# Optimization experiments

Measured on AMD Instinct MI355X. Metric: run time of the kernel, lower is better.

Reference implementation:

```python
import jax, jax.numpy as jnp
import numpy as np

HEADS = 8


def setup_inputs() -> dict:
    key = jax.random.key(0)
    ks = jax.random.split(key, 5)
    B, C, H, W = 4, 256, 48, 48
    x = jax.random.normal(ks[0], (B, C, H, W), dtype=jnp.float32)
    # 1x1 conv weights == channel matmul matrices
    w_qkv = jax.random.normal(ks[1], (3 * C, C), dtype=jnp.float32) * (C ** -0.5)
    b_qkv = jax.random.normal(ks[2], (3 * C,), dtype=jnp.float32) * 0.02
    w_proj = jax.random.normal(ks[3], (C, C), dtype=jnp.float32) * (C ** -0.5)
    b_proj = jax.random.normal(ks[4], (C,), dtype=jnp.float32) * 0.02
    return {"x": x, "w_qkv": w_qkv, "b_qkv": b_qkv, "w_proj": w_proj, "b_proj": b_proj}


def reference(x, w_qkv, b_qkv, w_proj, b_proj):
    B, C, H, W = x.shape
    heads = HEADS
    dh = C // heads
    HW = H * W
    scale = dh ** -0.5
    # qkv 1x1 conv: [B, 3C, H, W]
    qkv = jnp.einsum('bchw,oc->bohw', x, w_qkv) + b_qkv[None, :, None, None]
    # reshape(B,3,heads,dh,HW).transpose(-2,-1) -> [B,3,heads,HW,dh]
    qkv = qkv.reshape(B, 3, heads, dh, HW).transpose(0, 1, 2, 4, 3)
    q = qkv[:, 0] * scale  # [B,h,HW,dh]
    k = qkv[:, 1]
    v = qkv[:, 2]
    scores = jnp.einsum('bhnd,bhmd->bhnm', q, k)  # [B,h,HW,HW]
    scores = scores - jnp.max(scores, axis=-1, keepdims=True)
    exp_scores = jnp.exp(scores)
    weights = exp_scores / jnp.maximum(exp_scores.sum(axis=-1, keepdims=True), 1e-12)
    attn = jnp.einsum('bhnm,bhmd->bhnd', weights, v)  # [B,h,HW,dh]
    # transpose(2,3).reshape(B,C,H,W): [B,h,dh,HW] -> [B,C,H,W]
    attn = attn.transpose(0, 1, 3, 2).reshape(B, C, H, W)
    out = jnp.einsum('bchw,oc->bohw', attn, w_proj) + b_proj[None, :, None, None]
    return out
```

## Files before the change

kernel.cpp:

```cpp
#include <hip/hip_runtime.h>
#include <math.h>

#define HW 2304
#define QS 0.2550565355f

typedef _Float16 f16;
typedef __attribute__((ext_vector_type(4))) _Float16 f16x4;
typedef __attribute__((ext_vector_type(8))) _Float16 f16x8;
typedef __attribute__((ext_vector_type(4))) float f32x4;

#if __has_builtin(__builtin_amdgcn_exp2f)
#define EXP2F(x) __builtin_amdgcn_exp2f(x)
#else
#define EXP2F(x) exp2f(x)
#endif

static __device__ __forceinline__ f16x4 pack4(float a, float b, float c, float d) {
    auto lo = __builtin_amdgcn_cvt_pkrtz(a, b);
    auto hi = __builtin_amdgcn_cvt_pkrtz(c, d);
    f16x4 r;
    r[0] = (f16)lo[0]; r[1] = (f16)lo[1]; r[2] = (f16)hi[0]; r[3] = (f16)hi[1];
    return r;
}

__global__ __launch_bounds__(256) void cvt_w(const float* __restrict__ wq,
                                             const float* __restrict__ wp,
                                             f16* __restrict__ wh) {
    const int i = (blockIdx.x * 256 + threadIdx.x) * 4;
    float4 v;
    if (i < 768 * 256) v = *(const float4*)(wq + i);
    else               v = *(const float4*)(wp + (i - 768 * 256));
    f16x4 h = {(f16)v.x, (f16)v.y, (f16)v.z, (f16)v.w};
    *(f16x4*)(wh + i) = h;
}

__global__ __launch_bounds__(256) void cvt_x(const float* __restrict__ x,
                                             f16* __restrict__ xt) {
    __shared__ f16 tile[64][72];
    const int t  = threadIdx.x;
    const int n0 = blockIdx.x * 64, c0 = blockIdx.y * 64, b = blockIdx.z;
    const float* xb = x + ((size_t)b * 256 + c0) * HW + n0;
#pragma unroll
    for (int pass = 0; pass < 4; ++pass) {
        const int u  = t + pass * 256;
        const int cr = u >> 4, cc = u & 15;
        const float4 v = *(const float4*)(xb + (size_t)cr * HW + 4 * cc);
        tile[4 * cc + 0][cr] = (f16)v.x;
        tile[4 * cc + 1][cr] = (f16)v.y;
        tile[4 * cc + 2][cr] = (f16)v.z;
        tile[4 * cc + 3][cr] = (f16)v.w;
    }
    __syncthreads();
    f16* xo = xt + ((size_t)b * HW + n0) * 256 + c0;
#pragma unroll
    for (int pass = 0; pass < 2; ++pass) {
        const int u  = t + pass * 256;
        const int nr = u >> 3, nc = u & 7;
        *(f16x8*)(xo + (size_t)nr * 256 + 8 * nc) = *(const f16x8*)&tile[nr][8 * nc];
    }
}

__global__ __launch_bounds__(64) void qkv_gemm(const f16* __restrict__ xt,
                                               const f16* __restrict__ wh,
                                               const float* __restrict__ bias,
                                               f16* __restrict__ qt,
                                               f16* __restrict__ kt,
                                               f16* __restrict__ vn) {
    const int lane = threadIdx.x & 63;
    const int c    = lane & 15, q4 = lane >> 4;
    const int n0   = blockIdx.x * 64;
    const int m0   = blockIdx.y * 64;
    const int b    = blockIdx.z;
    const int s    = (blockIdx.x + blockIdx.y) & 7;
    const f16* xb  = xt + (size_t)b * HW * 256;

    f32x4 C[4][4] = {};
    f16x8 af[2][4], bf[2][4];
    const int k0 = s * 32;
#pragma unroll
    for (int mt = 0; mt < 4; ++mt)
        af[0][mt] = *(const f16x8*)(wh + (size_t)(m0 + mt * 16 + c) * 256 + k0 + q4 * 8);
#pragma unroll
    for (int nt = 0; nt < 4; ++nt)
        bf[0][nt] = *(const f16x8*)(xb + (size_t)(n0 + nt * 16 + c) * 256 + k0 + q4 * 8);

#pragma unroll
    for (int it = 0; it < 8; ++it) {
        const int p = it & 1, pn = p ^ 1;
        const int kn = ((s + it + 1) & 7) * 32;
#pragma unroll
        for (int mt = 0; mt < 4; ++mt)
            af[pn][mt] = *(const f16x8*)(wh + (size_t)(m0 + mt * 16 + c) * 256 + kn + q4 * 8);
#pragma unroll
        for (int nt = 0; nt < 4; ++nt)
            bf[pn][nt] = *(const f16x8*)(xb + (size_t)(n0 + nt * 16 + c) * 256 + kn + q4 * 8);
#pragma unroll
        for (int mt = 0; mt < 4; ++mt)
#pragma unroll
            for (int nt = 0; nt < 4; ++nt)
                C[mt][nt] = __builtin_amdgcn_mfma_f32_16x16x32_f16(af[p][mt], bf[p][nt], C[mt][nt], 0, 0, 0);
    }

#pragma unroll
    for (int mt = 0; mt < 4; ++mt) {
        const int od = m0 + mt * 16 + q4 * 4;
        const float4 bv = *(const float4*)(bias + od);
        const int seg = od >> 8;
        const int oo  = od & 255;
        const int h   = oo >> 5, d0 = oo & 31;
        const size_t bh = (size_t)b * 8 + h;
#pragma unroll
        for (int nt = 0; nt < 4; ++nt) {
            const int n = n0 + nt * 16 + c;
            float v0 = C[mt][nt][0] + bv.x;
            float v1 = C[mt][nt][1] + bv.y;
            float v2 = C[mt][nt][2] + bv.z;
            float v3 = C[mt][nt][3] + bv.w;
            if (seg == 0) {
                v0 *= QS; v1 *= QS; v2 *= QS; v3 *= QS;
                f16x4 hv = {(f16)v0, (f16)v1, (f16)v2, (f16)v3};
                *(f16x4*)(qt + (bh * HW + n) * 32 + d0) = hv;
            } else if (seg == 1) {
                f16x4 hv = {(f16)v0, (f16)v1, (f16)v2, (f16)v3};
                *(f16x4*)(kt + (bh * HW + n) * 32 + d0) = hv;
            } else {
                const int nsw = n0 + (c >> 2) * 16 + nt * 4 + (c & 3);
                vn[(bh * 32 + d0 + 0) * HW + nsw] = (f16)v0;
                vn[(bh * 32 + d0 + 1) * HW + nsw] = (f16)v1;
                vn[(bh * 32 + d0 + 2) * HW + nsw] = (f16)v2;
                vn[(bh * 32 + d0 + 3) * HW + nsw] = (f16)v3;
            }
        }
    }
}

__global__ __launch_bounds__(256, 3) void attn_kernel(const f16* __restrict__ qt,
                                                      const f16* __restrict__ kt,
                                                      const f16* __restrict__ vn,
                                                      f16* __restrict__ at) {
    __shared__ float ored[2][96][36];
    __shared__ float lred[2][96];

    const int t    = threadIdx.x;
    const int lane = t & 63;
    const int w    = t >> 6;
    const int gh   = w >> 1;
    const int jh   = w & 1;
    const int c    = lane & 15, q4 = lane >> 4;
    const int bhid = blockIdx.x;
    const int h    = bhid & 7, b = bhid >> 3;
    const int i0   = blockIdx.y * 96;
    const size_t bh = (size_t)b * 8 + h;

    const f16* qtb = qt + bh * (size_t)HW * 32;
    const f16* kb = kt + bh * (size_t)HW * 32 + (size_t)(jh * 1152 + c) * 32 + q4 * 8;
    const f16* vb = vn + bh * (size_t)32 * HW + (size_t)c * HW + jh * 1152 + q4 * 16;

    f16x8 qf[3];
#pragma unroll
    for (int g = 0; g < 3; ++g)
        qf[g] = *(const f16x8*)(qtb + (size_t)(i0 + gh * 48 + g * 16 + c) * 32 + q4 * 8);

    const f16 oneh = (f16)(c == 0 ? 1.0f : 0.0f);
    const f16x4 ones = {oneh, oneh, oneh, oneh};

    f32x4 O[3][2] = {};
    f32x4 lacc[3] = {};

    f16x8 kA[4], kB[4];
    f16x4 vA[2][4], vB[2][4];

#define LOADK(dst, j) {                                                        \
        const f16* p_ = kb + (size_t)(j) * 32;                                 \
        dst[0] = *(const f16x8*)(p_);                                          \
        dst[1] = *(const f16x8*)(p_ + 512);                                    \
        dst[2] = *(const f16x8*)(p_ + 1024);                                   \
        dst[3] = *(const f16x8*)(p_ + 1536);                                   \
    }
#define LOADV(dst, j) {                                                        \
        const f16* p_ = vb + (j);                                              \
        *(f16x8*)&dst[0][0] = *(const f16x8*)(p_);                             \
        *(f16x8*)&dst[0][2] = *(const f16x8*)(p_ + 8);                         \
        *(f16x8*)&dst[1][0] = *(const f16x8*)(p_ + 16 * HW);                   \
        *(f16x8*)&dst[1][2] = *(const f16x8*)(p_ + 16 * HW + 8);               \
    }
#define COMPUTE(kf, vv) {                                                      \
        const f32x4 z_ = {0.f, 0.f, 0.f, 0.f};                                 \
        _Pragma("unroll")                                                      \
        for (int t4 = 0; t4 < 4; ++t4) {                                       \
            f16x4 P[3];                                                        \
            _Pragma("unroll")                                                  \
            for (int g = 0; g < 3; ++g) {                                      \
                const f32x4 S = __builtin_amdgcn_mfma_f32_16x16x32_f16(        \
                    kf[t4], qf[g], z_, 0, 0, 0);                               \
                P[g] = pack4(EXP2F(S[0]), EXP2F(S[1]), EXP2F(S[2]),            \
                             EXP2F(S[3]));                                     \
            }                                                                  \
            _Pragma("unroll")                                                  \
            for (int g = 0; g < 3; ++g) {                                      \
                O[g][0] = __builtin_amdgcn_mfma_f32_16x16x16f16(               \
                    vv[0][t4], P[g], O[g][0], 0, 0, 0);                        \
                O[g][1] = __builtin_amdgcn_mfma_f32_16x16x16f16(               \
                    vv[1][t4], P[g], O[g][1], 0, 0, 0);                        \
                lacc[g] = __builtin_amdgcn_mfma_f32_16x16x16f16(               \
                    ones, P[g], lacc[g], 0, 0, 0);                             \
            }                                                                  \
        }                                                                      \
    }

    LOADK(kA, 0);
    LOADV(vA, 0);
#pragma unroll 1
    for (int s = 0; s < 9; ++s) {
        const int j1 = s * 128 + 64;
        const int j2 = (s == 8) ? 0 : j1 + 64;
        LOADK(kB, j1);
        LOADV(vB, j1);
        COMPUTE(kA, vA);
        LOADK(kA, j2);
        LOADV(vA, j2);
        COMPUTE(kB, vB);
    }
#undef LOADK
#undef LOADV
#undef COMPUTE

#pragma unroll
    for (int g = 0; g < 3; ++g) {
        const int row = gh * 48 + g * 16 + c;
#pragma unroll
        for (int dh = 0; dh < 2; ++dh)
            *(f32x4*)&ored[jh][row][dh * 16 + q4 * 4] = O[g][dh];
        if (q4 == 0) lred[jh][row] = lacc[g][0];
    }
    __syncthreads();

    if (t < 192) {
        const int i   = t >> 1;
        const int d16 = (t & 1) * 16;
        const float l = lred[0][i] + lred[1][i];
        const float inv = 1.f / fmaxf(l, 1e-12f);
        float4 s[4];
#pragma unroll
        for (int k = 0; k < 4; ++k) {
            const float4 pa = *(const float4*)&ored[0][i][d16 + 4 * k];
            const float4 pb = *(const float4*)&ored[1][i][d16 + 4 * k];
            s[k].x = pa.x + pb.x; s[k].y = pa.y + pb.y;
            s[k].z = pa.z + pb.z; s[k].w = pa.w + pb.w;
        }
        f16* op = at + ((size_t)b * HW + i0 + i) * 256 + h * 32 + d16;
        *(f16x4*)(op + 0)  = pack4(s[0].x * inv, s[0].y * inv, s[0].z * inv, s[0].w * inv);
        *(f16x4*)(op + 4)  = pack4(s[1].x * inv, s[1].y * inv, s[1].z * inv, s[1].w * inv);
        *(f16x4*)(op + 8)  = pack4(s[2].x * inv, s[2].y * inv, s[2].z * inv, s[2].w * inv);
        *(f16x4*)(op + 12) = pack4(s[3].x * inv, s[3].y * inv, s[3].z * inv, s[3].w * inv);
    }
}

__global__ __launch_bounds__(64) void proj_gemm(const f16* __restrict__ at,
                                                const f16* __restrict__ wh,
                                                const float* __restrict__ bias,
                                                float* __restrict__ out) {
    const int lane = threadIdx.x & 63;
    const int c    = lane & 15, q4 = lane >> 4;
    const int n0   = blockIdx.x * 64;
    const int m0   = blockIdx.y * 64;
    const int b    = blockIdx.z;
    const int s    = (blockIdx.x + blockIdx.y) & 7;
    const f16* ab  = at + (size_t)b * HW * 256;

    f32x4 C[4][4] = {};
    f16x8 af[2][4], bf[2][4];
    const int k0 = s * 32;
#pragma unroll
    for (int mt = 0; mt < 4; ++mt)
        af[0][mt] = *(const f16x8*)(wh + (size_t)(m0 + mt * 16 + c) * 256 + k0 + q4 * 8);
#pragma unroll
    for (int nt = 0; nt < 4; ++nt)
        bf[0][nt] = *(const f16x8*)(ab + (size_t)(n0 + nt * 16 + c) * 256 + k0 + q4 * 8);

#pragma unroll
    for (int it = 0; it < 8; ++it) {
        const int p = it & 1, pn = p ^ 1;
        const int kn = ((s + it + 1) & 7) * 32;
#pragma unroll
        for (int mt = 0; mt < 4; ++mt)
            af[pn][mt] = *(const f16x8*)(wh + (size_t)(m0 + mt * 16 + c) * 256 + kn + q4 * 8);
#pragma unroll
        for (int nt = 0; nt < 4; ++nt)
            bf[pn][nt] = *(const f16x8*)(ab + (size_t)(n0 + nt * 16 + c) * 256 + kn + q4 * 8);
#pragma unroll
        for (int mt = 0; mt < 4; ++mt)
#pragma unroll
            for (int nt = 0; nt < 4; ++nt)
                C[mt][nt] = __builtin_amdgcn_mfma_f32_16x16x32_f16(af[p][mt], bf[p][nt], C[mt][nt], 0, 0, 0);
    }

#pragma unroll
    for (int mt = 0; mt < 4; ++mt) {
        const int od = m0 + mt * 16 + q4 * 4;
        const float4 bv = *(const float4*)(bias + od);
#pragma unroll
        for (int nt = 0; nt < 4; ++nt) {
            const int n = n0 + nt * 16 + c;
            out[((size_t)b * 256 + od + 0) * HW + n] = C[mt][nt][0] + bv.x;
            out[((size_t)b * 256 + od + 1) * HW + n] = C[mt][nt][1] + bv.y;
            out[((size_t)b * 256 + od + 2) * HW + n] = C[mt][nt][2] + bv.z;
            out[((size_t)b * 256 + od + 3) * HW + n] = C[mt][nt][3] + bv.w;
        }
    }
}

extern "C" void kernel_launch(void* const* d_in, const int* in_sizes, int n_in,
                              void* d_out, int out_size, void* d_ws, size_t ws_size,
                              hipStream_t stream) {
    const float* x      = (const float*)d_in[0];
    const float* w_qkv  = (const float*)d_in[1];
    const float* b_qkv  = (const float*)d_in[2];
    const float* w_proj = (const float*)d_in[3];
    const float* b_proj = (const float*)d_in[4];
    float* out = (float*)d_out;

    const size_t per = (size_t)4 * HW * 256;
    f16* xt = (f16*)d_ws;
    f16* wh = xt + per;
    f16* qt = wh + 262144;
    f16* kt = qt + per;
    f16* vn = kt + per;
    f16* at = vn + per;

    cvt_w<<<256, 256, 0, stream>>>(w_qkv, w_proj, wh);
    cvt_x<<<dim3(36, 4, 4), 256, 0, stream>>>(x, xt);
    qkv_gemm<<<dim3(36, 12, 4), 64, 0, stream>>>(xt, wh, b_qkv, qt, kt, vn);
    attn_kernel<<<dim3(32, 24), 256, 0, stream>>>(qt, kt, vn, at);
    proj_gemm<<<dim3(36, 4, 4), 64, 0, stream>>>(at, wh + 768 * 256, b_proj, out);
}
```

Measured before the change: 144.0 us.

## Stage K/V tiles through LDS in attention; merge conversion kernels; drop k-rotation

In the attention kernel, the four waves cooperatively load K and V tiles into double-buffered shared memory instead of each wave reading its own copy straight from global memory. This removes redundant global loads across waves that share the same j-half. The cost is a barrier per tile and extra LDS traffic. The two fp32-to-fp16 conversion kernels are merged into one launch, and the staggered k-start rotation in the GEMMs is replaced by plain sequential k order.

```diff
diff --git a/kernel.cpp b/kernel.cpp
--- a/kernel.cpp
+++ b/kernel.cpp
@@ -23,22 +23,26 @@
     return r;
 }
 
-__global__ __launch_bounds__(256) void cvt_w(const float* __restrict__ wq,
-                                             const float* __restrict__ wp,
-                                             f16* __restrict__ wh) {
-    const int i = (blockIdx.x * 256 + threadIdx.x) * 4;
-    float4 v;
-    if (i < 768 * 256) v = *(const float4*)(wq + i);
-    else               v = *(const float4*)(wp + (i - 768 * 256));
-    f16x4 h = {(f16)v.x, (f16)v.y, (f16)v.z, (f16)v.w};
-    *(f16x4*)(wh + i) = h;
-}
-
-__global__ __launch_bounds__(256) void cvt_x(const float* __restrict__ x,
-                                             f16* __restrict__ xt) {
+__global__ __launch_bounds__(256) void cvt_all(const float* __restrict__ x,
+                                               const float* __restrict__ wq,
+                                               const float* __restrict__ wp,
+                                               f16* __restrict__ xt,
+                                               f16* __restrict__ wh) {
     __shared__ f16 tile[64][72];
-    const int t  = threadIdx.x;
-    const int n0 = blockIdx.x * 64, c0 = blockIdx.y * 64, b = blockIdx.z;
+    const int bid = blockIdx.x;
+    const int t   = threadIdx.x;
+    if (bid >= 576) {
+        const int i = ((bid - 576) * 256 + t) * 4;
+        float4 v;
+        if (i < 768 * 256) v = *(const float4*)(wq + i);
+        else               v = *(const float4*)(wp + (i - 768 * 256));
+        f16x4 h = {(f16)v.x, (f16)v.y, (f16)v.z, (f16)v.w};
+        *(f16x4*)(wh + i) = h;
+        return;
+    }
+    const int bx = bid % 36, rem = bid / 36;
+    const int by = rem & 3, bz = rem >> 2;
+    const int n0 = bx * 64, c0 = by * 64, b = bz;
     const float* xb = x + ((size_t)b * 256 + c0) * HW + n0;
 #pragma unroll
     for (int pass = 0; pass < 4; ++pass) {
@@ -71,23 +75,21 @@
     const int n0   = blockIdx.x * 64;
     const int m0   = blockIdx.y * 64;
     const int b    = blockIdx.z;
-    const int s    = (blockIdx.x + blockIdx.y) & 7;
     const f16* xb  = xt + (size_t)b * HW * 256;
 
     f32x4 C[4][4] = {};
     f16x8 af[2][4], bf[2][4];
-    const int k0 = s * 32;
 #pragma unroll
     for (int mt = 0; mt < 4; ++mt)
-        af[0][mt] = *(const f16x8*)(wh + (size_t)(m0 + mt * 16 + c) * 256 + k0 + q4 * 8);
+        af[0][mt] = *(const f16x8*)(wh + (size_t)(m0 + mt * 16 + c) * 256 + q4 * 8);
 #pragma unroll
     for (int nt = 0; nt < 4; ++nt)
-        bf[0][nt] = *(const f16x8*)(xb + (size_t)(n0 + nt * 16 + c) * 256 + k0 + q4 * 8);
+        bf[0][nt] = *(const f16x8*)(xb + (size_t)(n0 + nt * 16 + c) * 256 + q4 * 8);
 
 #pragma unroll
     for (int it = 0; it < 8; ++it) {
         const int p = it & 1, pn = p ^ 1;
-        const int kn = ((s + it + 1) & 7) * 32;
+        const int kn = (it == 7) ? 0 : (it + 1) * 32;
 #pragma unroll
         for (int mt = 0; mt < 4; ++mt)
             af[pn][mt] = *(const f16x8*)(wh + (size_t)(m0 + mt * 16 + c) * 256 + kn + q4 * 8);
@@ -138,14 +140,17 @@
                                                       const f16* __restrict__ kt,
                                                       const f16* __restrict__ vn,
                                                       f16* __restrict__ at) {
-    __shared__ float ored[2][96][36];
-    __shared__ float lred[2][96];
+    __shared__ __align__(16) char smem[34816];
+    f16* Kls = (f16*)smem;
+    f16* Vls = (f16*)(smem + 16384);
 
     const int t    = threadIdx.x;
     const int lane = t & 63;
     const int w    = t >> 6;
     const int gh   = w >> 1;
     const int jh   = w & 1;
+    const int sv   = w >> 1;
+    const int shf  = w & 1;
     const int c    = lane & 15, q4 = lane >> 4;
     const int bhid = blockIdx.x;
     const int h    = bhid & 7, b = bhid >> 3;
@@ -153,8 +158,8 @@
     const size_t bh = (size_t)b * 8 + h;
 
     const f16* qtb = qt + bh * (size_t)HW * 32;
-    const f16* kb = kt + bh * (size_t)HW * 32 + (size_t)(jh * 1152 + c) * 32 + q4 * 8;
-    const f16* vb = vn + bh * (size_t)32 * HW + (size_t)c * HW + jh * 1152 + q4 * 16;
+    const f16* ktb = kt + bh * (size_t)HW * 32;
+    const f16* vnb = vn + bh * (size_t)32 * HW;
 
     f16x8 qf[3];
 #pragma unroll
@@ -167,24 +172,57 @@
     f32x4 O[3][2] = {};
     f32x4 lacc[3] = {};
 
-    f16x8 kA[4], kB[4];
-    f16x4 vA[2][4], vB[2][4];
-
-#define LOADK(dst, j) {                                                        \
-        const f16* p_ = kb + (size_t)(j) * 32;                                 \
-        dst[0] = *(const f16x8*)(p_);                                          \
-        dst[1] = *(const f16x8*)(p_ + 512);                                    \
-        dst[2] = *(const f16x8*)(p_ + 1024);                                   \
-        dst[3] = *(const f16x8*)(p_ + 1536);                                   \
-    }
-#define LOADV(dst, j) {                                                        \
-        const f16* p_ = vb + (j);                                              \
-        *(f16x8*)&dst[0][0] = *(const f16x8*)(p_);                             \
-        *(f16x8*)&dst[0][2] = *(const f16x8*)(p_ + 8);                         \
-        *(f16x8*)&dst[1][0] = *(const f16x8*)(p_ + 16 * HW);                   \
-        *(f16x8*)&dst[1][2] = *(const f16x8*)(p_ + 16 * HW + 8);               \
-    }
-#define COMPUTE(kf, vv) {                                                      \
+    const f16* ksrc = ktb + (size_t)(shf * 1152 + (lane >> 2)) * 32 + (lane & 3) * 8;
+    const f16* vsrc = vnb + (size_t)(lane & 31) * HW + shf * 1152 + (lane >> 5) * 8;
+    const int kdoff = (lane >> 2) * 32 + (lane & 3) * 8;
+    const int vdoff = (lane & 31) * 72 + (lane >> 5) * 8;
+
+    f16x8 sreg[4];
+
+#define STAGE_LOAD(jn) {                                                       \
+        if (sv == 0) {                                                         \
+            const f16* p_ = ksrc + (size_t)(jn) * 32;                          \
+            sreg[0] = *(const f16x8*)(p_);                                     \
+            sreg[1] = *(const f16x8*)(p_ + 512);                               \
+            sreg[2] = *(const f16x8*)(p_ + 1024);                              \
+            sreg[3] = *(const f16x8*)(p_ + 1536);                              \
+        } else {                                                               \
+            const f16* p_ = vsrc + (jn);                                       \
+            sreg[0] = *(const f16x8*)(p_);                                     \
+            sreg[1] = *(const f16x8*)(p_ + 16);                                \
+            sreg[2] = *(const f16x8*)(p_ + 32);                                \
+            sreg[3] = *(const f16x8*)(p_ + 48);                                \
+        }                                                                      \
+    }
+#define STAGE_WRITE(nb) {                                                      \
+        if (sv == 0) {                                                         \
+            f16* d_ = Kls + ((nb) * 2 + shf) * 2048 + kdoff;                   \
+            *(f16x8*)(d_)        = sreg[0];                                    \
+            *(f16x8*)(d_ + 512)  = sreg[1];                                    \
+            *(f16x8*)(d_ + 1024) = sreg[2];                                    \
+            *(f16x8*)(d_ + 1536) = sreg[3];                                    \
+        } else {                                                               \
+            f16* d_ = Vls + ((nb) * 2 + shf) * 2304 + vdoff;                   \
+            *(f16x8*)(d_)      = sreg[0];                                      \
+            *(f16x8*)(d_ + 16) = sreg[1];                                      \
+            *(f16x8*)(d_ + 32) = sreg[2];                                      \
+            *(f16x8*)(d_ + 48) = sreg[3];                                      \
+        }                                                                      \
+    }
+#define COMPUTE(cb) {                                                          \
+        const f16* Kt = Kls + ((cb) * 2 + jh) * 2048;                          \
+        const f16* Vt = Vls + ((cb) * 2 + jh) * 2304;                          \
+        f16x8 kf[4];                                                           \
+        f16x4 vv[2][4];                                                        \
+        _Pragma("unroll")                                                      \
+        for (int t4 = 0; t4 < 4; ++t4)                                         \
+            kf[t4] = *(const f16x8*)(Kt + (t4 * 16 + c) * 32 + q4 * 8);        \
+        _Pragma("unroll")                                                      \
+        for (int dh = 0; dh < 2; ++dh) {                                       \
+            const f16* vp = Vt + (dh * 16 + c) * 72 + q4 * 16;                 \
+            *(f16x8*)&vv[dh][0] = *(const f16x8*)(vp);                         \
+            *(f16x8*)&vv[dh][2] = *(const f16x8*)(vp + 8);                     \
+        }                                                                      \
         const f32x4 z_ = {0.f, 0.f, 0.f, 0.f};                                 \
         _Pragma("unroll")                                                      \
         for (int t4 = 0; t4 < 4; ++t4) {                                       \
@@ -208,22 +246,25 @@
         }                                                                      \
     }
 
-    LOADK(kA, 0);
-    LOADV(vA, 0);
+    STAGE_LOAD(0);
+    STAGE_WRITE(0);
+    __syncthreads();
+
 #pragma unroll 1
-    for (int s = 0; s < 9; ++s) {
-        const int j1 = s * 128 + 64;
-        const int j2 = (s == 8) ? 0 : j1 + 64;
-        LOADK(kB, j1);
-        LOADV(vB, j1);
-        COMPUTE(kA, vA);
-        LOADK(kA, j2);
-        LOADV(vA, j2);
-        COMPUTE(kB, vB);
-    }
-#undef LOADK
-#undef LOADV
+    for (int tt = 0; tt < 18; ++tt) {
+        const int cur = tt & 1, nxt = cur ^ 1;
+        const int jn = (tt == 17) ? 0 : (tt + 1) * 64;
+        STAGE_LOAD(jn);
+        COMPUTE(cur);
+        STAGE_WRITE(nxt);
+        __syncthreads();
+    }
+#undef STAGE_LOAD
+#undef STAGE_WRITE
 #undef COMPUTE
+
+    float (*ored)[96][36] = (float (*)[96][36])(smem);
+    float (*lred)[96]     = (float (*)[96])(smem + 27648);
 
 #pragma unroll
     for (int g = 0; g < 3; ++g) {
@@ -265,23 +306,21 @@
     const int n0   = blockIdx.x * 64;
     const int m0   = blockIdx.y * 64;
     const int b    = blockIdx.z;
-    const int s    = (blockIdx.x + blockIdx.y) & 7;
     const f16* ab  = at + (size_t)b * HW * 256;
 
     f32x4 C[4][4] = {};
     f16x8 af[2][4], bf[2][4];
-    const int k0 = s * 32;
 #pragma unroll
     for (int mt = 0; mt < 4; ++mt)
-        af[0][mt] = *(const f16x8*)(wh + (size_t)(m0 + mt * 16 + c) * 256 + k0 + q4 * 8);
+        af[0][mt] = *(const f16x8*)(wh + (size_t)(m0 + mt * 16 + c) * 256 + q4 * 8);
 #pragma unroll
     for (int nt = 0; nt < 4; ++nt)
-        bf[0][nt] = *(const f16x8*)(ab + (size_t)(n0 + nt * 16 + c) * 256 + k0 + q4 * 8);
+        bf[0][nt] = *(const f16x8*)(ab + (size_t)(n0 + nt * 16 + c) * 256 + q4 * 8);
 
 #pragma unroll
     for (int it = 0; it < 8; ++it) {
         const int p = it & 1, pn = p ^ 1;
-        const int kn = ((s + it + 1) & 7) * 32;
+        const int kn = (it == 7) ? 0 : (it + 1) * 32;
 #pragma unroll
         for (int mt = 0; mt < 4; ++mt)
             af[pn][mt] = *(const f16x8*)(wh + (size_t)(m0 + mt * 16 + c) * 256 + kn + q4 * 8);
@@ -328,8 +367,7 @@
     f16* vn = kt + per;
     f16* at = vn + per;
 
-    cvt_w<<<256, 256, 0, stream>>>(w_qkv, w_proj, wh);
-    cvt_x<<<dim3(36, 4, 4), 256, 0, stream>>>(x, xt);
+    cvt_all<<<832, 256, 0, stream>>>(x, w_qkv, w_proj, xt, wh);
     qkv_gemm<<<dim3(36, 12, 4), 64, 0, stream>>>(xt, wh, b_qkv, qt, kt, vn);
     attn_kernel<<<dim3(32, 24), 256, 0, stream>>>(qt, kt, vn, at);
     proj_gemm<<<dim3(36, 4, 4), 64, 0, stream>>>(at, wh + 768 * 256, b_proj, out);
```

Measured after the change: 133.1 us. -7.6%, faster.
